# Kernel optimization log

Hardware: AMD Instinct MI355X
Metric: run time of the kernel (lower is better)

## Reference

```python
import jax, jax.numpy as jnp
import numpy as np

B, S, D, H = 4, 1024, 1024, 16
HD = D // H  # head_dim = 64


def setup_inputs() -> dict:
    key = jax.random.key(0)
    ks = jax.random.split(key, 9)
    scale = jnp.float32(1.0 / np.sqrt(D))
    w = lambda k: jax.random.normal(k, (D, D), jnp.float32) * scale
    return {
        "x": jax.random.normal(ks[0], (B, S, D), jnp.float32),
        "Wq_r": w(ks[1]), "Wq_i": w(ks[2]),
        "Wk_r": w(ks[3]), "Wk_i": w(ks[4]),
        "Wv_r": w(ks[5]), "Wv_i": w(ks[6]),
        "Wo_r": w(ks[7]), "Wo_i": w(ks[8]),
        "mask": jnp.ones((B, S, S), dtype=bool),
    }


def reference(x, Wq_r, Wq_i, Wk_r, Wk_i, Wv_r, Wv_i, Wo_r, Wo_i, mask):
    # Optical encoding: magnitude * exp(i * angle(x + i*roll(x,1,-1)))
    mag = jnp.abs(x)
    phase = jnp.arctan2(jnp.roll(x, 1, axis=-1), x)  # angle(x + i*rolled)
    opt = (mag * jnp.cos(phase)) + 1j * (mag * jnp.sin(phase))  # complex64 [B,S,D]

    Wq = Wq_r + 1j * Wq_i
    Wk = Wk_r + 1j * Wk_i
    Wv = Wv_r + 1j * Wv_i
    Wo = Wo_r + 1j * Wo_i

    def heads(t):  # [B,S,D] -> [B,H,S,HD]
        return jnp.transpose(t.reshape(B, S, H, HD), (0, 2, 1, 3))

    Q = heads(opt @ Wq)
    K = heads(opt @ Wk)
    V = heads(opt @ Wv)

    # Photonic correlation: abs of complex dot Q . conj(K)
    corr = jnp.einsum('bhqd,bhkd->bhqk', Q, jnp.conj(K))
    scores = jnp.abs(corr) / jnp.sqrt(jnp.float32(HD))
    scores = jnp.where(mask[:, None, :, :], scores, -jnp.inf)
    attn = jax.nn.softmax(scores, axis=-1)  # real weights [B,H,S,S]

    out = jnp.einsum('bhqk,bhkd->bhqd', attn.astype(V.dtype), V)  # complex
    out = jnp.transpose(out, (0, 2, 1, 3)).reshape(B, S, D)
    return jnp.real(out @ Wo)
```

## Files before the change

### kernel.cpp

```cpp
#include <hip/hip_runtime.h>
#include <hip/hip_bf16.h>


#define BB 4
#define SS 1024
#define DD 1024
#define HH 16
#define HD 64

typedef _Float16 f16x8 __attribute__((ext_vector_type(8)));
typedef _Float16 f16x4 __attribute__((ext_vector_type(4)));
typedef float    f32x4 __attribute__((ext_vector_type(4)));
typedef int      i32x2 __attribute__((ext_vector_type(2)));
typedef unsigned int u32x4 __attribute__((ext_vector_type(4)));

#define LOG2E 1.44269504f
#define C8S 0.18033688f

__global__ __launch_bounds__(256) void k_encode_h(const float* __restrict__ x,
                                                  _Float16* __restrict__ ore,
                                                  _Float16* __restrict__ oim) {
    const int g   = blockIdx.x * 256 + threadIdx.x;
    const int row = g >> 8;
    const int d0  = (g & 255) * 4;
    const float* xr = x + (size_t)row * DD;
    const float4 xc = *(const float4*)(xr + d0);
    const float xp0 = xr[(d0 + DD - 1) & (DD - 1)];
    const float cv[4] = {xc.x, xc.y, xc.z, xc.w};
    const float pv[4] = {xp0, xc.x, xc.y, xc.z};
    f16x4 hr, hi;
    #pragma unroll
    for (int j = 0; j < 4; ++j) {
        const float r2 = cv[j]*cv[j] + pv[j]*pv[j];
        float re = 0.f, im = 0.f;
        if (r2 > 1e-30f) {
            const float inv = rsqrtf(r2);
            const float mag = fabsf(cv[j]);
            re = mag * cv[j] * inv;
            im = mag * pv[j] * inv;
        }
        hr[j] = (_Float16)re; hi[j] = (_Float16)im;
    }
    *(f16x4*)(ore + (size_t)row*DD + d0) = hr;
    *(f16x4*)(oim + (size_t)row*DD + d0) = hi;
}

__global__ __launch_bounds__(256) void k_transw8(
    const float* w0, const float* w1, const float* w2, const float* w3,
    const float* w4, const float* w5, const float* w6, const float* w7,
    _Float16* wt)
{
    __shared__ _Float16 tile[64][68];
    const float* W;
    switch (blockIdx.z) {
        case 0: W = w0; break; case 1: W = w1; break;
        case 2: W = w2; break; case 3: W = w3; break;
        case 4: W = w4; break; case 5: W = w5; break;
        case 6: W = w6; break; default: W = w7; break;
    }
    _Float16* Wt = wt + (size_t)blockIdx.z * (1u << 20);
    const int t = threadIdx.x;
    const int r = t >> 4, c4 = (t & 15) * 4;
    const int gx = blockIdx.x * 64, gy = blockIdx.y * 64;
    #pragma unroll
    for (int rr = 0; rr < 4; ++rr) {
        const float4 v = *(const float4*)(W + (size_t)(gy + r + rr*16)*DD + gx + c4);
        tile[r + rr*16][c4+0] = (_Float16)v.x;
        tile[r + rr*16][c4+1] = (_Float16)v.y;
        tile[r + rr*16][c4+2] = (_Float16)v.z;
        tile[r + rr*16][c4+3] = (_Float16)v.w;
    }
    __syncthreads();
    #pragma unroll
    for (int rr = 0; rr < 4; ++rr) {
        const int n = r + rr*16;
        f16x4 o;
        o[0] = tile[c4+0][n]; o[1] = tile[c4+1][n];
        o[2] = tile[c4+2][n]; o[3] = tile[c4+3][n];
        *(f16x4*)(Wt + (size_t)(gx + n)*DD + gy + c4) = o;
    }
}

template<int MODE>
__global__ __launch_bounds__(256, 2) void k_cgemm_h(
    const _Float16* __restrict__ Ar, const _Float16* __restrict__ Ai,
    const _Float16* __restrict__ Btr, const _Float16* __restrict__ Bti,
    _Float16* __restrict__ Cr, _Float16* __restrict__ Ci, float* __restrict__ Cf)
{
    __shared__ _Float16 lds[2][4][4096];

    const int t = threadIdx.x, w = t >> 6, l = t & 63;
    const int lr = l & 15, lg = l >> 4;

    int wg = blockIdx.x;
    wg = (wg & 7) * 32 + (wg >> 3);
    const int m0 = (wg >> 3) * 128;
    const int n0 = (wg & 7) * 128;
    const int wr = w >> 1, wc = w & 1;

    const _Float16* gbase = (w == 0) ? Ar : (w == 1) ? Ai : (w == 2) ? Btr : Bti;
    const int rowbase = (w < 2) ? m0 : n0;
    const _Float16* gp = gbase + (size_t)(rowbase + (l >> 2)) * 1024 + (l & 3) * 8;

    #define GSTAGE(K0_, BUF_)                                                         \
        {                                                                             \
            _Float16* lb = &lds[BUF_][w][0];                                          \
            _Pragma("unroll")                                                         \
            for (int i = 0; i < 8; ++i)                                               \
                __builtin_amdgcn_global_load_lds(                                     \
                    (const __attribute__((address_space(1))) void*)                   \
                        (gp + (size_t)i*16*1024 + (K0_)),                             \
                    (__attribute__((address_space(3))) void*)(lb + i*512), 16, 0, 0); \
        }

    f32x4 accR[4][4] = {};
    f32x4 accI[4][4] = {};

    GSTAGE(0, 0);
    int cur = 0;

    for (int kt = 0; kt < 32; ++kt) {
        if (kt < 31) {
            GSTAGE((kt + 1) * 32, cur ^ 1);
            asm volatile("s_waitcnt vmcnt(8)" ::: "memory");
        } else {
            asm volatile("s_waitcnt vmcnt(0)" ::: "memory");
        }
        __builtin_amdgcn_s_barrier();
        __builtin_amdgcn_sched_barrier(0);

        const _Float16* lA = &lds[cur][0][0] + (wr*64 + lr)*32 + lg*8;
        const _Float16* lB = &lds[cur][2][0] + (wc*64 + lr)*32 + lg*8;

        f16x8 ar[4], ai[4], br[4], bi[4], nai[4];
        #pragma unroll
        for (int i = 0; i < 4; ++i) {
            ar[i] = *(const f16x8*)(lA + i*512);
            ai[i] = *(const f16x8*)(lA + 4096 + i*512);
            br[i] = *(const f16x8*)(lB + i*512);
            bi[i] = *(const f16x8*)(lB + 4096 + i*512);
            union { f16x8 h; u32x4 u; } nx;
            nx.h = ai[i]; nx.u ^= 0x80008000u; nai[i] = nx.h;
        }
        __builtin_amdgcn_s_setprio(1);
        #pragma unroll
        for (int i = 0; i < 4; ++i) {
            #pragma unroll
            for (int j = 0; j < 4; ++j) {
                accR[i][j] = __builtin_amdgcn_mfma_f32_16x16x32_f16(ar[i],  br[j], accR[i][j], 0, 0, 0);
                accR[i][j] = __builtin_amdgcn_mfma_f32_16x16x32_f16(nai[i], bi[j], accR[i][j], 0, 0, 0);
                if (MODE == 0) {
                    accI[i][j] = __builtin_amdgcn_mfma_f32_16x16x32_f16(ar[i], bi[j], accI[i][j], 0, 0, 0);
                    accI[i][j] = __builtin_amdgcn_mfma_f32_16x16x32_f16(ai[i], br[j], accI[i][j], 0, 0, 0);
                }
            }
        }
        __builtin_amdgcn_s_setprio(0);
        __builtin_amdgcn_sched_barrier(0);
        __builtin_amdgcn_s_barrier();
        cur ^= 1;
    }

    #pragma unroll
    for (int i = 0; i < 4; ++i) {
        #pragma unroll
        for (int j = 0; j < 4; ++j) {
            const int m = m0 + wr*64 + i*16 + lg*4;
            const int n = n0 + wc*64 + j*16 + lr;
            #pragma unroll
            for (int r = 0; r < 4; ++r) {
                if (MODE == 0) {
                    Cr[(size_t)(m + r)*1024 + n] = (_Float16)accR[i][j][r];
                    Ci[(size_t)(m + r)*1024 + n] = (_Float16)accI[i][j][r];
                } else {
                    Cf[(size_t)(m + r)*1024 + n] = accR[i][j][r];
                }
            }
        }
    }
}

#define QB 64
#define KT 32

__global__ __launch_bounds__(256, 4) void k_attn6(
    const _Float16* Qre, const _Float16* Qim,
    const _Float16* __restrict__ Kre, const _Float16* __restrict__ Kim,
    const _Float16* __restrict__ Vre, const _Float16* __restrict__ Vim,
    _Float16* Ore, _Float16* Oim)
{
    __shared__ __align__(16) _Float16 lds[2][4][2048];

    const int t = threadIdx.x, w = t >> 6, l = t & 63;
    const int lr = l & 15, lg = l >> 4;
    const int bh = blockIdx.x;
    const int h = bh & (HH - 1), b = bh >> 4;
    const int qw = blockIdx.y * QB + w * 16;

    const size_t kvbase = ((size_t)(b * SS)) * DD + h * HD;

    f16x8 qr[2], qi[2], nqr[2];
    {
        const size_t qoff = ((size_t)(b*SS + qw + lr)) * DD + h*HD + lg*8;
        #pragma unroll
        for (int ks = 0; ks < 2; ++ks) {
            qr[ks] = *(const f16x8*)(Qre + qoff + 32*ks);
            qi[ks] = *(const f16x8*)(Qim + qoff + 32*ks);
            union { f16x8 h; u32x4 u; } nx;
            nx.h = qr[ks]; nx.u ^= 0x80008000u; nqr[ks] = nx.h;
        }
    }

    const _Float16* gsrc;
    if (w < 2)
        gsrc = ((w == 0) ? Kre : Kim) + kvbase + (size_t)(l >> 3) * DD + ((l & 7) ^ (l >> 3)) * 8;
    else
        gsrc = ((w == 2) ? Vre : Vim) + kvbase + (size_t)(l >> 1) * DD + (l & 1) * 8;

    #define STAGE(KT_, BUF_)                                                          \
        {                                                                             \
            _Float16* lb = &lds[BUF_][w][0];                                          \
            if (w < 2) {                                                              \
                _Pragma("unroll")                                                     \
                for (int i = 0; i < 4; ++i)                                           \
                    __builtin_amdgcn_global_load_lds(                                 \
                        (const __attribute__((address_space(1))) void*)               \
                            (gsrc + (size_t)((KT_)*KT + 8*i) * DD),                   \
                        (__attribute__((address_space(3))) void*)(lb + i*512),        \
                        16, 0, 0);                                                    \
            } else {                                                                  \
                _Pragma("unroll")                                                     \
                for (int i = 0; i < 4; ++i)                                           \
                    __builtin_amdgcn_global_load_lds(                                 \
                        (const __attribute__((address_space(1))) void*)               \
                            (gsrc + (size_t)((KT_)*KT) * DD + i*16),                  \
                        (__attribute__((address_space(3))) void*)(lb + i*512),        \
                        16, 0, 0);                                                    \
            }                                                                         \
        }

    f32x4 o_re[4] = {}, o_im[4] = {};
    float m_s  = 32.f;
    float m2_s = 1024.f;
    float mC_s = -32.f * C8S;
    float l_l  = 0.f;

    STAGE(0, 0);
    int cur = 0;

    for (int kt = 0; kt < SS/KT; ++kt) {
        if (kt < SS/KT - 1) {
            STAGE(kt + 1, cur ^ 1);
            asm volatile("s_waitcnt vmcnt(4)" ::: "memory");
        } else {
            asm volatile("s_waitcnt vmcnt(0)" ::: "memory");
        }
        __builtin_amdgcn_s_barrier();
        __builtin_amdgcn_sched_barrier(0);

        const _Float16* Kr_s = &lds[cur][0][0];
        const _Float16* Ki_s = &lds[cur][1][0];

        f32x4 dre[2] = {}, dim_[2] = {};
        #pragma unroll
        for (int st = 0; st < 2; ++st) {
            const int row = st*16 + lr;
            #pragma unroll
            for (int ks = 0; ks < 2; ++ks) {
                const int c = ((4*ks + lg) ^ (lr & 7)) * 8;
                const f16x8 kr = *(const f16x8*)(Kr_s + row*64 + c);
                const f16x8 ki = *(const f16x8*)(Ki_s + row*64 + c);
                dre[st]  = __builtin_amdgcn_mfma_f32_16x16x32_f16(kr, qr[ks],  dre[st],  0, 0, 0);
                dre[st]  = __builtin_amdgcn_mfma_f32_16x16x32_f16(ki, qi[ks],  dre[st],  0, 0, 0);
                dim_[st] = __builtin_amdgcn_mfma_f32_16x16x32_f16(kr, qi[ks],  dim_[st], 0, 0, 0);
                dim_[st] = __builtin_amdgcn_mfma_f32_16x16x32_f16(ki, nqr[ks], dim_[st], 0, 0, 0);
            }
        }

        f16x4 pa[2];
        {
            float d2[2][4];
            float t2 = 0.f;
            #pragma unroll
            for (int st = 0; st < 2; ++st)
                #pragma unroll
                for (int r = 0; r < 4; ++r) {
                    d2[st][r] = fmaf(dre[st][r], dre[st][r],
                                     dim_[st][r] * dim_[st][r]);
                    t2 = fmaxf(t2, d2[st][r]);
                }
            if (!__all(t2 <= m2_s)) {
                float tm;
                asm("v_sqrt_f32 %0, %1" : "=v"(tm) : "v"(t2));
                tm = fmaxf(tm, __shfl_xor(tm, 16));
                tm = fmaxf(tm, __shfl_xor(tm, 32));
                const float mn = fmaxf(m_s, tm);
                const float ce = (m_s - mn) * C8S;
                float cq;
                asm("v_exp_f32 %0, %1" : "=v"(cq) : "v"(ce));
                l_l *= cq;
                f32x4 cT;
                #pragma unroll
                for (int r = 0; r < 4; ++r) cT[r] = __shfl(cq, lg*4 + r);
                #pragma unroll
                for (int d = 0; d < 4; ++d) { o_re[d] *= cT; o_im[d] *= cT; }
                m_s  = mn;
                m2_s = mn * mn;
                mC_s = -mn * C8S;
            }
            float ls = 0.f;
            #pragma unroll
            for (int st = 0; st < 2; ++st)
                #pragma unroll
                for (int r = 0; r < 4; ++r) {
                    float u, p;
                    asm("v_sqrt_f32 %0, %1" : "=v"(u) : "v"(d2[st][r]));
                    const float e = fmaf(u, C8S, mC_s);
                    asm("v_exp_f32 %0, %1" : "=v"(p) : "v"(e));
                    pa[st][r] = (_Float16)p;
                    ls += p;
                }
            l_l += ls;
        }

        const unsigned vrb = (unsigned)(uintptr_t)&lds[cur][2][0] + 8u*l;
        const unsigned vib = (unsigned)(uintptr_t)&lds[cur][3][0] + 8u*l;
        i32x2 fr[2][2], fi[2][2];
        #pragma unroll
        for (int st = 0; st < 2; ++st) {
            asm volatile("ds_read_b64_tr_b16 %0, %1" : "=v"(fr[0][st]) : "v"(vrb + st*512u) : "memory");
            asm volatile("ds_read_b64_tr_b16 %0, %1" : "=v"(fi[0][st]) : "v"(vib + st*512u) : "memory");
        }
        #pragma unroll
        for (int d = 0; d < 4; ++d) {
            const int cb = d & 1, nb = cb ^ 1;
            if (d < 3) {
                #pragma unroll
                for (int st = 0; st < 2; ++st) {
                    asm volatile("ds_read_b64_tr_b16 %0, %1" : "=v"(fr[nb][st]) : "v"(vrb + (d+1)*1024u + st*512u) : "memory");
                    asm volatile("ds_read_b64_tr_b16 %0, %1" : "=v"(fi[nb][st]) : "v"(vib + (d+1)*1024u + st*512u) : "memory");
                }
                asm volatile("s_waitcnt lgkmcnt(4)" ::: "memory");
            } else {
                asm volatile("s_waitcnt lgkmcnt(0)" ::: "memory");
            }
            __builtin_amdgcn_sched_barrier(0);
            __builtin_amdgcn_s_setprio(1);
            #pragma unroll
            for (int st = 0; st < 2; ++st) {
                union { i32x2 i; f16x4 h; } cr_, ci_;
                cr_.i = fr[cb][st]; ci_.i = fi[cb][st];
                o_re[d] = __builtin_amdgcn_mfma_f32_16x16x16f16(pa[st], cr_.h, o_re[d], 0, 0, 0);
                o_im[d] = __builtin_amdgcn_mfma_f32_16x16x16f16(pa[st], ci_.h, o_im[d], 0, 0, 0);
            }
            __builtin_amdgcn_s_setprio(0);
        }

        __builtin_amdgcn_sched_barrier(0);
        __builtin_amdgcn_s_barrier();
        cur ^= 1;
    }

    {
        float lq = l_l;
        lq += __shfl_xor(lq, 16);
        lq += __shfl_xor(lq, 32);
        const float inv = 1.f / lq;
        f32x4 iT;
        #pragma unroll
        for (int r = 0; r < 4; ++r) iT[r] = __shfl(inv, lg*4 + r);
        #pragma unroll
        for (int d = 0; d < 4; ++d)
            #pragma unroll
            for (int r = 0; r < 4; ++r) {
                const size_t row = (size_t)(b*SS + qw + lg*4 + r);
                Ore[row*DD + h*HD + d*16 + lr] = (_Float16)(o_re[d][r] * iT[r]);
                Oim[row*DD + h*HD + d*16 + lr] = (_Float16)(o_im[d][r] * iT[r]);
            }
    }
}

extern "C" void kernel_launch(void* const* d_in, const int* in_sizes, int n_in,
                              void* d_out, int out_size, void* d_ws, size_t ws_size,
                              hipStream_t stream) {
    const float* x   = (const float*)d_in[0];
    const float* Wqr = (const float*)d_in[1];
    const float* Wqi = (const float*)d_in[2];
    const float* Wkr = (const float*)d_in[3];
    const float* Wki = (const float*)d_in[4];
    const float* Wvr = (const float*)d_in[5];
    const float* Wvi = (const float*)d_in[6];
    const float* Wor = (const float*)d_in[7];
    const float* Woi = (const float*)d_in[8];

    const size_t P  = (size_t)BB * SS * DD;
    const size_t WP = 1u << 20;
    if (ws_size < (8 * P + 8 * WP) * sizeof(_Float16)) return;

    _Float16* wh   = (_Float16*)d_ws;
    _Float16* optR = wh;
    _Float16* optI = wh + P;
    _Float16* Qr = wh + 2*P; _Float16* Qi = wh + 3*P;
    _Float16* Kr = wh + 4*P; _Float16* Ki = wh + 5*P;
    _Float16* Vr = wh + 6*P; _Float16* Vi = wh + 7*P;
    _Float16* W8 = wh + 8*P;

    k_encode_h<<<(int)(P / 1024), 256, 0, stream>>>(x, optR, optI);
    k_transw8<<<dim3(16, 16, 8), 256, 0, stream>>>(Wqr, Wqi, Wkr, Wki, Wvr, Wvi, Wor, Woi, W8);

    k_cgemm_h<0><<<256, 256, 0, stream>>>(optR, optI, W8 + 0*WP, W8 + 1*WP, Qr, Qi, nullptr);
    k_cgemm_h<0><<<256, 256, 0, stream>>>(optR, optI, W8 + 2*WP, W8 + 3*WP, Kr, Ki, nullptr);
    k_cgemm_h<0><<<256, 256, 0, stream>>>(optR, optI, W8 + 4*WP, W8 + 5*WP, Vr, Vi, nullptr);

    k_attn6<<<dim3(BB * HH, SS / QB, 1), 256, 0, stream>>>(Qr, Qi, Kr, Ki, Vr, Vi, Qr, Qi);

    k_cgemm_h<1><<<256, 256, 0, stream>>>(Qr, Qi, W8 + 6*WP, W8 + 7*WP,
                                          nullptr, nullptr, (float*)d_out);
}
```

Before: 242.2 us.

## Fuse QKV GEMMs into one launch and split attention over key halves

The three Q/K/V complex GEMM launches are merged into one 768-block launch that picks the weight matrix from the block index. Attention is split along the key dimension into two halves (grid z=2), doubling the block count for better CU occupancy. Each half writes unnormalised partial outputs plus row max and sum, and a new combine kernel merges them with log-sum-exp rescaling. The output GEMM becomes its own kernel specialised for the real part. The cost is extra workspace, an extra launch, and more fp16 partial-output traffic, with some precision risk from storing unnormalised partials in fp16.

```diff
diff --git a/kernel.cpp b/kernel.cpp
--- a/kernel.cpp
+++ b/kernel.cpp
@@ -81,22 +81,29 @@
     }
 }
 
-template<int MODE>
-__global__ __launch_bounds__(256, 2) void k_cgemm_h(
+__global__ __launch_bounds__(256, 2) void k_cgemm_qkv(
     const _Float16* __restrict__ Ar, const _Float16* __restrict__ Ai,
-    const _Float16* __restrict__ Btr, const _Float16* __restrict__ Bti,
-    _Float16* __restrict__ Cr, _Float16* __restrict__ Ci, float* __restrict__ Cf)
+    const _Float16* __restrict__ W8, _Float16* __restrict__ CQ)
 {
     __shared__ _Float16 lds[2][4][4096];
 
     const int t = threadIdx.x, w = t >> 6, l = t & 63;
     const int lr = l & 15, lg = l >> 4;
+    const size_t P  = (size_t)BB * SS * DD;
+    const size_t WP = 1u << 20;
 
     int wg = blockIdx.x;
-    wg = (wg & 7) * 32 + (wg >> 3);
-    const int m0 = (wg >> 3) * 128;
-    const int n0 = (wg & 7) * 128;
+    wg = (wg & 7) * 96 + (wg >> 3);
+    const int mt  = wg / 24, nt = wg % 24;
+    const int m0  = mt * 128;
+    const int mat = nt >> 3;
+    const int n0  = (nt & 7) * 128;
     const int wr = w >> 1, wc = w & 1;
+
+    const _Float16* Btr = W8 + (size_t)mat * 2 * WP;
+    const _Float16* Bti = Btr + WP;
+    _Float16* Cr = CQ + (size_t)mat * 2 * P;
+    _Float16* Ci = Cr + P;
 
     const _Float16* gbase = (w == 0) ? Ar : (w == 1) ? Ai : (w == 2) ? Btr : Bti;
     const int rowbase = (w < 2) ? m0 : n0;
@@ -149,10 +156,8 @@
             for (int j = 0; j < 4; ++j) {
                 accR[i][j] = __builtin_amdgcn_mfma_f32_16x16x32_f16(ar[i],  br[j], accR[i][j], 0, 0, 0);
                 accR[i][j] = __builtin_amdgcn_mfma_f32_16x16x32_f16(nai[i], bi[j], accR[i][j], 0, 0, 0);
-                if (MODE == 0) {
-                    accI[i][j] = __builtin_amdgcn_mfma_f32_16x16x32_f16(ar[i], bi[j], accI[i][j], 0, 0, 0);
-                    accI[i][j] = __builtin_amdgcn_mfma_f32_16x16x32_f16(ai[i], br[j], accI[i][j], 0, 0, 0);
-                }
+                accI[i][j] = __builtin_amdgcn_mfma_f32_16x16x32_f16(ar[i],  bi[j], accI[i][j], 0, 0, 0);
+                accI[i][j] = __builtin_amdgcn_mfma_f32_16x16x32_f16(ai[i],  br[j], accI[i][j], 0, 0, 0);
             }
         }
         __builtin_amdgcn_s_setprio(0);
@@ -169,13 +174,85 @@
             const int n = n0 + wc*64 + j*16 + lr;
             #pragma unroll
             for (int r = 0; r < 4; ++r) {
-                if (MODE == 0) {
-                    Cr[(size_t)(m + r)*1024 + n] = (_Float16)accR[i][j][r];
-                    Ci[(size_t)(m + r)*1024 + n] = (_Float16)accI[i][j][r];
-                } else {
-                    Cf[(size_t)(m + r)*1024 + n] = accR[i][j][r];
-                }
-            }
+                Cr[(size_t)(m + r)*1024 + n] = (_Float16)accR[i][j][r];
+                Ci[(size_t)(m + r)*1024 + n] = (_Float16)accI[i][j][r];
+            }
+        }
+    }
+}
+
+__global__ __launch_bounds__(256, 2) void k_cgemm_o(
+    const _Float16* __restrict__ Ar, const _Float16* __restrict__ Ai,
+    const _Float16* __restrict__ Btr, const _Float16* __restrict__ Bti,
+    float* __restrict__ Cf)
+{
+    __shared__ _Float16 lds[2][4][4096];
+
+    const int t = threadIdx.x, w = t >> 6, l = t & 63;
+    const int lr = l & 15, lg = l >> 4;
+
+    int wg = blockIdx.x;
+    wg = (wg & 7) * 32 + (wg >> 3);
+    const int m0 = (wg >> 3) * 128;
+    const int n0 = (wg & 7) * 128;
+    const int wr = w >> 1, wc = w & 1;
+
+    const _Float16* gbase = (w == 0) ? Ar : (w == 1) ? Ai : (w == 2) ? Btr : Bti;
+    const int rowbase = (w < 2) ? m0 : n0;
+    const _Float16* gp = gbase + (size_t)(rowbase + (l >> 2)) * 1024 + (l & 3) * 8;
+
+    f32x4 accR[4][4] = {};
+
+    GSTAGE(0, 0);
+    int cur = 0;
+
+    for (int kt = 0; kt < 32; ++kt) {
+        if (kt < 31) {
+            GSTAGE((kt + 1) * 32, cur ^ 1);
+            asm volatile("s_waitcnt vmcnt(8)" ::: "memory");
+        } else {
+            asm volatile("s_waitcnt vmcnt(0)" ::: "memory");
+        }
+        __builtin_amdgcn_s_barrier();
+        __builtin_amdgcn_sched_barrier(0);
+
+        const _Float16* lA = &lds[cur][0][0] + (wr*64 + lr)*32 + lg*8;
+        const _Float16* lB = &lds[cur][2][0] + (wc*64 + lr)*32 + lg*8;
+
+        f16x8 ar[4], br[4], bi[4], nai[4];
+        #pragma unroll
+        for (int i = 0; i < 4; ++i) {
+            ar[i] = *(const f16x8*)(lA + i*512);
+            f16x8 aiv = *(const f16x8*)(lA + 4096 + i*512);
+            br[i] = *(const f16x8*)(lB + i*512);
+            bi[i] = *(const f16x8*)(lB + 4096 + i*512);
+            union { f16x8 h; u32x4 u; } nx;
+            nx.h = aiv; nx.u ^= 0x80008000u; nai[i] = nx.h;
+        }
+        __builtin_amdgcn_s_setprio(1);
+        #pragma unroll
+        for (int i = 0; i < 4; ++i) {
+            #pragma unroll
+            for (int j = 0; j < 4; ++j) {
+                accR[i][j] = __builtin_amdgcn_mfma_f32_16x16x32_f16(ar[i],  br[j], accR[i][j], 0, 0, 0);
+                accR[i][j] = __builtin_amdgcn_mfma_f32_16x16x32_f16(nai[i], bi[j], accR[i][j], 0, 0, 0);
+            }
+        }
+        __builtin_amdgcn_s_setprio(0);
+        __builtin_amdgcn_sched_barrier(0);
+        __builtin_amdgcn_s_barrier();
+        cur ^= 1;
+    }
+
+    #pragma unroll
+    for (int i = 0; i < 4; ++i) {
+        #pragma unroll
+        for (int j = 0; j < 4; ++j) {
+            const int m = m0 + wr*64 + i*16 + lg*4;
+            const int n = n0 + wc*64 + j*16 + lr;
+            #pragma unroll
+            for (int r = 0; r < 4; ++r)
+                Cf[(size_t)(m + r)*1024 + n] = accR[i][j][r];
         }
     }
 }
@@ -183,11 +260,11 @@
 #define QB 64
 #define KT 32
 
-__global__ __launch_bounds__(256, 4) void k_attn6(
-    const _Float16* Qre, const _Float16* Qim,
+__global__ __launch_bounds__(256, 4) void k_attn7(
+    const _Float16* __restrict__ Qre, const _Float16* __restrict__ Qim,
     const _Float16* __restrict__ Kre, const _Float16* __restrict__ Kim,
     const _Float16* __restrict__ Vre, const _Float16* __restrict__ Vim,
-    _Float16* Ore, _Float16* Oim)
+    _Float16* __restrict__ PO, float* __restrict__ Lb, float* __restrict__ Mb)
 {
     __shared__ __align__(16) _Float16 lds[2][4][2048];
 
@@ -196,6 +273,11 @@
     const int bh = blockIdx.x;
     const int h = bh & (HH - 1), b = bh >> 4;
     const int qw = blockIdx.y * QB + w * 16;
+    const int z  = blockIdx.z;
+    const int kt0 = z * 16, kt1 = kt0 + 16;
+    const size_t PLANE = (size_t)BB * SS * DD;
+    _Float16* Por = PO + (size_t)z * 2 * PLANE;
+    _Float16* Poi = Por + PLANE;
 
     const size_t kvbase = ((size_t)(b * SS)) * DD + h * HD;
 
@@ -245,11 +327,11 @@
     float mC_s = -32.f * C8S;
     float l_l  = 0.f;
 
-    STAGE(0, 0);
+    STAGE(kt0, 0);
     int cur = 0;
 
-    for (int kt = 0; kt < SS/KT; ++kt) {
-        if (kt < SS/KT - 1) {
+    for (int kt = kt0; kt < kt1; ++kt) {
+        if (kt < kt1 - 1) {
             STAGE(kt + 1, cur ^ 1);
             asm volatile("s_waitcnt vmcnt(4)" ::: "memory");
         } else {
@@ -365,19 +447,52 @@
         float lq = l_l;
         lq += __shfl_xor(lq, 16);
         lq += __shfl_xor(lq, 32);
-        const float inv = 1.f / lq;
-        f32x4 iT;
-        #pragma unroll
-        for (int r = 0; r < 4; ++r) iT[r] = __shfl(inv, lg*4 + r);
+        if (l < 16) {
+            const int q = qw + lr;
+            Lb[z * 65536 + (bh << 10) + q] = lq;
+            Mb[z * 65536 + (bh << 10) + q] = m_s;
+        }
         #pragma unroll
         for (int d = 0; d < 4; ++d)
             #pragma unroll
             for (int r = 0; r < 4; ++r) {
                 const size_t row = (size_t)(b*SS + qw + lg*4 + r);
-                Ore[row*DD + h*HD + d*16 + lr] = (_Float16)(o_re[d][r] * iT[r]);
-                Oim[row*DD + h*HD + d*16 + lr] = (_Float16)(o_im[d][r] * iT[r]);
-            }
-    }
+                Por[row*DD + h*HD + d*16 + lr] = (_Float16)o_re[d][r];
+                Poi[row*DD + h*HD + d*16 + lr] = (_Float16)o_im[d][r];
+            }
+    }
+}
+
+__global__ __launch_bounds__(256) void k_combine(
+    const _Float16* __restrict__ P0r, const _Float16* __restrict__ P0i,
+    const _Float16* __restrict__ P1r, const _Float16* __restrict__ P1i,
+    const float* __restrict__ Lb, const float* __restrict__ Mb,
+    _Float16* __restrict__ Or, _Float16* __restrict__ Oi)
+{
+    const int u = blockIdx.x * 256 + threadIdx.x;
+    const int row = u >> 7;
+    const int c8  = u & 127;
+    const int hh  = c8 >> 3;
+    const int q = row & 1023, b = row >> 10;
+    const int li = ((b * 16 + hh) << 10) + q;
+    const float l0 = Lb[li], l1 = Lb[65536 + li];
+    const float m0 = Mb[li], m1 = Mb[65536 + li];
+    const float mm = fmaxf(m0, m1);
+    const float f0 = exp2f((m0 - mm) * C8S);
+    const float f1 = exp2f((m1 - mm) * C8S);
+    const float inv = 1.f / fmaf(l0, f0, l1 * f1);
+    const float s0 = f0 * inv, s1 = f1 * inv;
+    const size_t off = (size_t)row * DD + c8 * 8;
+    const f16x8 a0 = *(const f16x8*)(P0r + off), a1 = *(const f16x8*)(P1r + off);
+    const f16x8 b0 = *(const f16x8*)(P0i + off), b1 = *(const f16x8*)(P1i + off);
+    f16x8 xr, xi;
+    #pragma unroll
+    for (int j = 0; j < 8; ++j) {
+        xr[j] = (_Float16)fmaf((float)a0[j], s0, (float)a1[j] * s1);
+        xi[j] = (_Float16)fmaf((float)b0[j], s0, (float)b1[j] * s1);
+    }
+    *(f16x8*)(Or + off) = xr;
+    *(f16x8*)(Oi + off) = xi;
 }
 
 extern "C" void kernel_launch(void* const* d_in, const int* in_sizes, int n_in,
@@ -395,7 +510,8 @@
 
     const size_t P  = (size_t)BB * SS * DD;
     const size_t WP = 1u << 20;
-    if (ws_size < (8 * P + 8 * WP) * sizeof(_Float16)) return;
+    const size_t need = (12 * P + 8 * WP) * sizeof(_Float16) + 4ull * 4 * 65536;
+    if (ws_size < need) return;
 
     _Float16* wh   = (_Float16*)d_ws;
     _Float16* optR = wh;
@@ -404,16 +520,21 @@
     _Float16* Kr = wh + 4*P; _Float16* Ki = wh + 5*P;
     _Float16* Vr = wh + 6*P; _Float16* Vi = wh + 7*P;
     _Float16* W8 = wh + 8*P;
+    _Float16* PO = wh + 8*P + 8*WP;
+    float*    LM = (float*)(wh + 12*P + 8*WP);
+    float*    Lb = LM;
+    float*    Mb = LM + 131072;
 
     k_encode_h<<<(int)(P / 1024), 256, 0, stream>>>(x, optR, optI);
     k_transw8<<<dim3(16, 16, 8), 256, 0, stream>>>(Wqr, Wqi, Wkr, Wki, Wvr, Wvi, Wor, Woi, W8);
 
-    k_cgemm_h<0><<<256, 256, 0, stream>>>(optR, optI, W8 + 0*WP, W8 + 1*WP, Qr, Qi, nullptr);
-    k_cgemm_h<0><<<256, 256, 0, stream>>>(optR, optI, W8 + 2*WP, W8 + 3*WP, Kr, Ki, nullptr);
-    k_cgemm_h<0><<<256, 256, 0, stream>>>(optR, optI, W8 + 4*WP, W8 + 5*WP, Vr, Vi, nullptr);
-
-    k_attn6<<<dim3(BB * HH, SS / QB, 1), 256, 0, stream>>>(Qr, Qi, Kr, Ki, Vr, Vi, Qr, Qi);
-
-    k_cgemm_h<1><<<256, 256, 0, stream>>>(Qr, Qi, W8 + 6*WP, W8 + 7*WP,
-                                          nullptr, nullptr, (float*)d_out);
-}
+    k_cgemm_qkv<<<768, 256, 0, stream>>>(optR, optI, W8, Qr);
+
+    k_attn7<<<dim3(BB * HH, SS / QB, 2), 256, 0, stream>>>(
+        Qr, Qi, Kr, Ki, Vr, Vi, PO, Lb, Mb);
+
+    k_combine<<<2048, 256, 0, stream>>>(PO, PO + P, PO + 2*P, PO + 3*P,
+                                        Lb, Mb, Qr, Qi);
+
+    k_cgemm_o<<<256, 256, 0, stream>>>(Qr, Qi, W8 + 6*WP, W8 + 7*WP, (float*)d_out);
+}
```

Result: faster. 228.7 us (-5.6%).

## Split attention over two KV halves with combine kernel; merge prep kernels

Applied to the files above, without the earlier changes.

Attention is now split along the key dimension into two halves (grid z=2). Each half writes unnormalized partial outputs plus row sums and maxima, and a new combine kernel rescales and merges the two halves before the output projection. This doubles the number of attention blocks, which raises occupancy on a grid that was only 1024 blocks. The cost is extra partial-output traffic, one more launch and more workspace. The encode and weight-transpose kernels are also fused into one launch to save launch overhead.

```diff
diff --git a/kernel.cpp b/kernel.cpp
--- a/kernel.cpp
+++ b/kernel.cpp
@@ -17,67 +17,69 @@
 #define LOG2E 1.44269504f
 #define C8S 0.18033688f
 
-__global__ __launch_bounds__(256) void k_encode_h(const float* __restrict__ x,
-                                                  _Float16* __restrict__ ore,
-                                                  _Float16* __restrict__ oim) {
-    const int g   = blockIdx.x * 256 + threadIdx.x;
-    const int row = g >> 8;
-    const int d0  = (g & 255) * 4;
-    const float* xr = x + (size_t)row * DD;
-    const float4 xc = *(const float4*)(xr + d0);
-    const float xp0 = xr[(d0 + DD - 1) & (DD - 1)];
-    const float cv[4] = {xc.x, xc.y, xc.z, xc.w};
-    const float pv[4] = {xp0, xc.x, xc.y, xc.z};
-    f16x4 hr, hi;
-    #pragma unroll
-    for (int j = 0; j < 4; ++j) {
-        const float r2 = cv[j]*cv[j] + pv[j]*pv[j];
-        float re = 0.f, im = 0.f;
-        if (r2 > 1e-30f) {
-            const float inv = rsqrtf(r2);
-            const float mag = fabsf(cv[j]);
-            re = mag * cv[j] * inv;
-            im = mag * pv[j] * inv;
-        }
-        hr[j] = (_Float16)re; hi[j] = (_Float16)im;
-    }
-    *(f16x4*)(ore + (size_t)row*DD + d0) = hr;
-    *(f16x4*)(oim + (size_t)row*DD + d0) = hi;
-}
-
-__global__ __launch_bounds__(256) void k_transw8(
+__global__ __launch_bounds__(256) void k_prep(
+    const float* __restrict__ x,
     const float* w0, const float* w1, const float* w2, const float* w3,
     const float* w4, const float* w5, const float* w6, const float* w7,
-    _Float16* wt)
+    _Float16* __restrict__ ore, _Float16* __restrict__ oim,
+    _Float16* __restrict__ wt)
 {
     __shared__ _Float16 tile[64][68];
-    const float* W;
-    switch (blockIdx.z) {
-        case 0: W = w0; break; case 1: W = w1; break;
-        case 2: W = w2; break; case 3: W = w3; break;
-        case 4: W = w4; break; case 5: W = w5; break;
-        case 6: W = w6; break; default: W = w7; break;
-    }
-    _Float16* Wt = wt + (size_t)blockIdx.z * (1u << 20);
     const int t = threadIdx.x;
-    const int r = t >> 4, c4 = (t & 15) * 4;
-    const int gx = blockIdx.x * 64, gy = blockIdx.y * 64;
-    #pragma unroll
-    for (int rr = 0; rr < 4; ++rr) {
-        const float4 v = *(const float4*)(W + (size_t)(gy + r + rr*16)*DD + gx + c4);
-        tile[r + rr*16][c4+0] = (_Float16)v.x;
-        tile[r + rr*16][c4+1] = (_Float16)v.y;
-        tile[r + rr*16][c4+2] = (_Float16)v.z;
-        tile[r + rr*16][c4+3] = (_Float16)v.w;
-    }
-    __syncthreads();
-    #pragma unroll
-    for (int rr = 0; rr < 4; ++rr) {
-        const int n = r + rr*16;
-        f16x4 o;
-        o[0] = tile[c4+0][n]; o[1] = tile[c4+1][n];
-        o[2] = tile[c4+2][n]; o[3] = tile[c4+3][n];
-        *(f16x4*)(Wt + (size_t)(gx + n)*DD + gy + c4) = o;
+
+    if (blockIdx.z < 8) {
+        const float* W;
+        switch (blockIdx.z) {
+            case 0: W = w0; break; case 1: W = w1; break;
+            case 2: W = w2; break; case 3: W = w3; break;
+            case 4: W = w4; break; case 5: W = w5; break;
+            case 6: W = w6; break; default: W = w7; break;
+        }
+        _Float16* Wt = wt + (size_t)blockIdx.z * (1u << 20);
+        const int r = t >> 4, c4 = (t & 15) * 4;
+        const int gx = blockIdx.x * 64, gy = blockIdx.y * 64;
+        #pragma unroll
+        for (int rr = 0; rr < 4; ++rr) {
+            const float4 v = *(const float4*)(W + (size_t)(gy + r + rr*16)*DD + gx + c4);
+            tile[r + rr*16][c4+0] = (_Float16)v.x;
+            tile[r + rr*16][c4+1] = (_Float16)v.y;
+            tile[r + rr*16][c4+2] = (_Float16)v.z;
+            tile[r + rr*16][c4+3] = (_Float16)v.w;
+        }
+        __syncthreads();
+        #pragma unroll
+        for (int rr = 0; rr < 4; ++rr) {
+            const int n = r + rr*16;
+            f16x4 o;
+            o[0] = tile[c4+0][n]; o[1] = tile[c4+1][n];
+            o[2] = tile[c4+2][n]; o[3] = tile[c4+3][n];
+            *(f16x4*)(Wt + (size_t)(gx + n)*DD + gy + c4) = o;
+        }
+    } else {
+        const int bid = (blockIdx.z - 8) * 256 + blockIdx.y * 16 + blockIdx.x;
+        const int g   = bid * 256 + t;
+        const int row = g >> 8;
+        const int d0  = (g & 255) * 4;
+        const float* xr = x + (size_t)row * DD;
+        const float4 xc = *(const float4*)(xr + d0);
+        const float xp0 = xr[(d0 + DD - 1) & (DD - 1)];
+        const float cv[4] = {xc.x, xc.y, xc.z, xc.w};
+        const float pv[4] = {xp0, xc.x, xc.y, xc.z};
+        f16x4 hr, hi;
+        #pragma unroll
+        for (int j = 0; j < 4; ++j) {
+            const float r2 = cv[j]*cv[j] + pv[j]*pv[j];
+            float re = 0.f, im = 0.f;
+            if (r2 > 1e-30f) {
+                const float inv = rsqrtf(r2);
+                const float mag = fabsf(cv[j]);
+                re = mag * cv[j] * inv;
+                im = mag * pv[j] * inv;
+            }
+            hr[j] = (_Float16)re; hi[j] = (_Float16)im;
+        }
+        *(f16x4*)(ore + (size_t)row*DD + d0) = hr;
+        *(f16x4*)(oim + (size_t)row*DD + d0) = hi;
     }
 }
 
@@ -183,11 +185,11 @@
 #define QB 64
 #define KT 32
 
-__global__ __launch_bounds__(256, 4) void k_attn6(
-    const _Float16* Qre, const _Float16* Qim,
+__global__ __launch_bounds__(256, 4) void k_attn7(
+    const _Float16* __restrict__ Qre, const _Float16* __restrict__ Qim,
     const _Float16* __restrict__ Kre, const _Float16* __restrict__ Kim,
     const _Float16* __restrict__ Vre, const _Float16* __restrict__ Vim,
-    _Float16* Ore, _Float16* Oim)
+    _Float16* __restrict__ PO, float* __restrict__ Lb, float* __restrict__ Mb)
 {
     __shared__ __align__(16) _Float16 lds[2][4][2048];
 
@@ -196,6 +198,11 @@
     const int bh = blockIdx.x;
     const int h = bh & (HH - 1), b = bh >> 4;
     const int qw = blockIdx.y * QB + w * 16;
+    const int z  = blockIdx.z;
+    const int kt0 = z * 16, kt1 = kt0 + 16;
+    const size_t PLANE = (size_t)BB * SS * DD;
+    _Float16* Por = PO + (size_t)z * 2 * PLANE;
+    _Float16* Poi = Por + PLANE;
 
     const size_t kvbase = ((size_t)(b * SS)) * DD + h * HD;
 
@@ -217,7 +224,7 @@
     else
         gsrc = ((w == 2) ? Vre : Vim) + kvbase + (size_t)(l >> 1) * DD + (l & 1) * 8;
 
-    #define STAGE(KT_, BUF_)                                                          \
+    #define ASTAGE(KT_, BUF_)                                                         \
         {                                                                             \
             _Float16* lb = &lds[BUF_][w][0];                                          \
             if (w < 2) {                                                              \
@@ -245,12 +252,12 @@
     float mC_s = -32.f * C8S;
     float l_l  = 0.f;
 
-    STAGE(0, 0);
+    ASTAGE(kt0, 0);
     int cur = 0;
 
-    for (int kt = 0; kt < SS/KT; ++kt) {
-        if (kt < SS/KT - 1) {
-            STAGE(kt + 1, cur ^ 1);
+    for (int kt = kt0; kt < kt1; ++kt) {
+        if (kt < kt1 - 1) {
+            ASTAGE(kt + 1, cur ^ 1);
             asm volatile("s_waitcnt vmcnt(4)" ::: "memory");
         } else {
             asm volatile("s_waitcnt vmcnt(0)" ::: "memory");
@@ -365,19 +372,52 @@
         float lq = l_l;
         lq += __shfl_xor(lq, 16);
         lq += __shfl_xor(lq, 32);
-        const float inv = 1.f / lq;
-        f32x4 iT;
-        #pragma unroll
-        for (int r = 0; r < 4; ++r) iT[r] = __shfl(inv, lg*4 + r);
+        if (l < 16) {
+            const int q = qw + lr;
+            Lb[z * 65536 + (bh << 10) + q] = lq;
+            Mb[z * 65536 + (bh << 10) + q] = m_s;
+        }
         #pragma unroll
         for (int d = 0; d < 4; ++d)
             #pragma unroll
             for (int r = 0; r < 4; ++r) {
                 const size_t row = (size_t)(b*SS + qw + lg*4 + r);
-                Ore[row*DD + h*HD + d*16 + lr] = (_Float16)(o_re[d][r] * iT[r]);
-                Oim[row*DD + h*HD + d*16 + lr] = (_Float16)(o_im[d][r] * iT[r]);
-            }
-    }
+                Por[row*DD + h*HD + d*16 + lr] = (_Float16)o_re[d][r];
+                Poi[row*DD + h*HD + d*16 + lr] = (_Float16)o_im[d][r];
+            }
+    }
+}
+
+__global__ __launch_bounds__(256) void k_combine(
+    const _Float16* __restrict__ P0r, const _Float16* __restrict__ P0i,
+    const _Float16* __restrict__ P1r, const _Float16* __restrict__ P1i,
+    const float* __restrict__ Lb, const float* __restrict__ Mb,
+    _Float16* __restrict__ Or, _Float16* __restrict__ Oi)
+{
+    const int u = blockIdx.x * 256 + threadIdx.x;
+    const int row = u >> 7;
+    const int c8  = u & 127;
+    const int hh  = c8 >> 3;
+    const int q = row & 1023, b = row >> 10;
+    const int li = ((b * 16 + hh) << 10) + q;
+    const float l0 = Lb[li], l1 = Lb[65536 + li];
+    const float m0 = Mb[li], m1 = Mb[65536 + li];
+    const float mm = fmaxf(m0, m1);
+    const float f0 = exp2f((m0 - mm) * C8S);
+    const float f1 = exp2f((m1 - mm) * C8S);
+    const float inv = 1.f / fmaf(l0, f0, l1 * f1);
+    const float s0 = f0 * inv, s1 = f1 * inv;
+    const size_t off = (size_t)row * DD + c8 * 8;
+    const f16x8 a0 = *(const f16x8*)(P0r + off), a1 = *(const f16x8*)(P1r + off);
+    const f16x8 b0 = *(const f16x8*)(P0i + off), b1 = *(const f16x8*)(P1i + off);
+    f16x8 xr, xi;
+    #pragma unroll
+    for (int j = 0; j < 8; ++j) {
+        xr[j] = (_Float16)fmaf((float)a0[j], s0, (float)a1[j] * s1);
+        xi[j] = (_Float16)fmaf((float)b0[j], s0, (float)b1[j] * s1);
+    }
+    *(f16x8*)(Or + off) = xr;
+    *(f16x8*)(Oi + off) = xi;
 }
 
 extern "C" void kernel_launch(void* const* d_in, const int* in_sizes, int n_in,
@@ -395,7 +435,8 @@
 
     const size_t P  = (size_t)BB * SS * DD;
     const size_t WP = 1u << 20;
-    if (ws_size < (8 * P + 8 * WP) * sizeof(_Float16)) return;
+    const size_t need = (12 * P + 8 * WP) * sizeof(_Float16) + 4ull * 4 * 65536;
+    if (ws_size < need) return;
 
     _Float16* wh   = (_Float16*)d_ws;
     _Float16* optR = wh;
@@ -404,15 +445,23 @@
     _Float16* Kr = wh + 4*P; _Float16* Ki = wh + 5*P;
     _Float16* Vr = wh + 6*P; _Float16* Vi = wh + 7*P;
     _Float16* W8 = wh + 8*P;
-
-    k_encode_h<<<(int)(P / 1024), 256, 0, stream>>>(x, optR, optI);
-    k_transw8<<<dim3(16, 16, 8), 256, 0, stream>>>(Wqr, Wqi, Wkr, Wki, Wvr, Wvi, Wor, Woi, W8);
+    _Float16* PO = wh + 8*P + 8*WP;
+    float*    LM = (float*)(wh + 12*P + 8*WP);
+    float*    Lb = LM;
+    float*    Mb = LM + 131072;
+
+    k_prep<<<dim3(16, 16, 24), 256, 0, stream>>>(
+        x, Wqr, Wqi, Wkr, Wki, Wvr, Wvi, Wor, Woi, optR, optI, W8);
 
     k_cgemm_h<0><<<256, 256, 0, stream>>>(optR, optI, W8 + 0*WP, W8 + 1*WP, Qr, Qi, nullptr);
     k_cgemm_h<0><<<256, 256, 0, stream>>>(optR, optI, W8 + 2*WP, W8 + 3*WP, Kr, Ki, nullptr);
     k_cgemm_h<0><<<256, 256, 0, stream>>>(optR, optI, W8 + 4*WP, W8 + 5*WP, Vr, Vi, nullptr);
 
-    k_attn6<<<dim3(BB * HH, SS / QB, 1), 256, 0, stream>>>(Qr, Qi, Kr, Ki, Vr, Vi, Qr, Qi);
+    k_attn7<<<dim3(BB * HH, SS / QB, 2), 256, 0, stream>>>(
+        Qr, Qi, Kr, Ki, Vr, Vi, PO, Lb, Mb);
+
+    k_combine<<<2048, 256, 0, stream>>>(PO, PO + P, PO + 2*P, PO + 3*P,
+                                        Lb, Mb, Qr, Qi);
 
     k_cgemm_h<1><<<256, 256, 0, stream>>>(Qr, Qi, W8 + 6*WP, W8 + 7*WP,
                                           nullptr, nullptr, (float*)d_out);
```

Result: slower. 251.4 us (+3.8%).

## Merge QKV projections into one launch and load B operands directly to registers

Applied to the files above, without the earlier changes.

The three Q/K/V complex GEMM launches become a single 768-block launch. Each block picks its weight matrix and output from its tile index, with a swizzle that groups blocks sharing the same A rows. Inside the GEMM, only the A operand is staged through LDS with async global-to-LDS copies, which halves LDS use. The B operand (transposed weights) is now loaded straight from global memory into double-buffered registers one step ahead. This removes launch gaps and improves A-tile reuse across the three weights, at the cost of more VGPR pressure and uncached-by-LDS B loads that could stall the MFMA loop.

```diff
diff --git a/kernel.cpp b/kernel.cpp
--- a/kernel.cpp
+++ b/kernel.cpp
@@ -82,83 +82,125 @@
 }
 
 template<int MODE>
-__global__ __launch_bounds__(256, 2) void k_cgemm_h(
+__global__ __launch_bounds__(256, 2) void k_cgemm_bd(
     const _Float16* __restrict__ Ar, const _Float16* __restrict__ Ai,
-    const _Float16* __restrict__ Btr, const _Float16* __restrict__ Bti,
-    _Float16* __restrict__ Cr, _Float16* __restrict__ Ci, float* __restrict__ Cf)
+    const _Float16* __restrict__ W8, _Float16* __restrict__ CQ,
+    float* __restrict__ Cf)
 {
-    __shared__ _Float16 lds[2][4][4096];
+    __shared__ _Float16 lds[2][2][4096];
 
     const int t = threadIdx.x, w = t >> 6, l = t & 63;
     const int lr = l & 15, lg = l >> 4;
-
-    int wg = blockIdx.x;
-    wg = (wg & 7) * 32 + (wg >> 3);
-    const int m0 = (wg >> 3) * 128;
-    const int n0 = (wg & 7) * 128;
+    const size_t P  = (size_t)BB * SS * DD;
+    const size_t WP = 1u << 20;
+
+    int m0, n0;
+    const _Float16* Btr;
+    const _Float16* Bti;
+    _Float16* Cr = nullptr; _Float16* Ci = nullptr;
+    if (MODE == 0) {
+        int wg = blockIdx.x;
+        wg = (wg & 7) * 96 + (wg >> 3);
+        const int mt = wg / 24, nt = wg % 24;
+        m0 = mt * 128;
+        const int mat = nt >> 3;
+        n0 = (nt & 7) * 128;
+        Btr = W8 + (size_t)mat * 2 * WP;
+        Bti = Btr + WP;
+        Cr = CQ + (size_t)mat * 2 * P;
+        Ci = Cr + P;
+    } else {
+        int wg = blockIdx.x;
+        wg = (wg & 7) * 32 + (wg >> 3);
+        m0 = (wg >> 3) * 128;
+        n0 = (wg & 7) * 128;
+        Btr = W8 + (size_t)6 * WP;
+        Bti = Btr + WP;
+    }
     const int wr = w >> 1, wc = w & 1;
 
-    const _Float16* gbase = (w == 0) ? Ar : (w == 1) ? Ai : (w == 2) ? Btr : Bti;
-    const int rowbase = (w < 2) ? m0 : n0;
-    const _Float16* gp = gbase + (size_t)(rowbase + (l >> 2)) * 1024 + (l & 3) * 8;
-
-    #define GSTAGE(K0_, BUF_)                                                         \
+    const _Float16* gsrc = ((w < 2) ? Ar : Ai)
+        + (size_t)(m0 + (w & 1) * 64 + (l >> 2)) * 1024 + (l & 3) * 8;
+    const int aseg = (w >> 1);
+    const int arow0 = (w & 1) * 64;
+
+    #define ASTG(K0_, BUF_)                                                           \
         {                                                                             \
-            _Float16* lb = &lds[BUF_][w][0];                                          \
+            _Float16* lb = &lds[BUF_][aseg][arow0 * 32];                              \
             _Pragma("unroll")                                                         \
-            for (int i = 0; i < 8; ++i)                                               \
+            for (int i = 0; i < 4; ++i)                                               \
                 __builtin_amdgcn_global_load_lds(                                     \
                     (const __attribute__((address_space(1))) void*)                   \
-                        (gp + (size_t)i*16*1024 + (K0_)),                             \
+                        (gsrc + (size_t)i*16*1024 + (K0_)),                           \
                     (__attribute__((address_space(3))) void*)(lb + i*512), 16, 0, 0); \
+        }
+
+    const size_t bbase = (size_t)(n0 + wc*64 + lr) * 1024 + lg * 8;
+
+    #define BLOAD(K0_, BR_, BI_)                                                      \
+        {                                                                             \
+            _Pragma("unroll")                                                         \
+            for (int j = 0; j < 4; ++j) {                                             \
+                const size_t o = bbase + (size_t)j*16*1024 + (K0_);                   \
+                BR_[j] = *(const f16x8*)(Btr + o);                                    \
+                BI_[j] = *(const f16x8*)(Bti + o);                                    \
+            }                                                                         \
         }
 
     f32x4 accR[4][4] = {};
     f32x4 accI[4][4] = {};
-
-    GSTAGE(0, 0);
-    int cur = 0;
-
-    for (int kt = 0; kt < 32; ++kt) {
-        if (kt < 31) {
-            GSTAGE((kt + 1) * 32, cur ^ 1);
-            asm volatile("s_waitcnt vmcnt(8)" ::: "memory");
-        } else {
-            asm volatile("s_waitcnt vmcnt(0)" ::: "memory");
-        }
-        __builtin_amdgcn_s_barrier();
-        __builtin_amdgcn_sched_barrier(0);
-
-        const _Float16* lA = &lds[cur][0][0] + (wr*64 + lr)*32 + lg*8;
-        const _Float16* lB = &lds[cur][2][0] + (wc*64 + lr)*32 + lg*8;
-
-        f16x8 ar[4], ai[4], br[4], bi[4], nai[4];
-        #pragma unroll
-        for (int i = 0; i < 4; ++i) {
-            ar[i] = *(const f16x8*)(lA + i*512);
-            ai[i] = *(const f16x8*)(lA + 4096 + i*512);
-            br[i] = *(const f16x8*)(lB + i*512);
-            bi[i] = *(const f16x8*)(lB + 4096 + i*512);
-            union { f16x8 h; u32x4 u; } nx;
-            nx.h = ai[i]; nx.u ^= 0x80008000u; nai[i] = nx.h;
-        }
-        __builtin_amdgcn_s_setprio(1);
-        #pragma unroll
-        for (int i = 0; i < 4; ++i) {
-            #pragma unroll
-            for (int j = 0; j < 4; ++j) {
-                accR[i][j] = __builtin_amdgcn_mfma_f32_16x16x32_f16(ar[i],  br[j], accR[i][j], 0, 0, 0);
-                accR[i][j] = __builtin_amdgcn_mfma_f32_16x16x32_f16(nai[i], bi[j], accR[i][j], 0, 0, 0);
-                if (MODE == 0) {
-                    accI[i][j] = __builtin_amdgcn_mfma_f32_16x16x32_f16(ar[i], bi[j], accI[i][j], 0, 0, 0);
-                    accI[i][j] = __builtin_amdgcn_mfma_f32_16x16x32_f16(ai[i], br[j], accI[i][j], 0, 0, 0);
-                }
-            }
-        }
-        __builtin_amdgcn_s_setprio(0);
-        __builtin_amdgcn_sched_barrier(0);
-        __builtin_amdgcn_s_barrier();
-        cur ^= 1;
+    f16x8 br0[4], bi0[4], br1[4], bi1[4];
+
+    ASTG(0, 0);
+    BLOAD(0, br0, bi0);
+
+    #define PHASE(KT_, CBUF_, NBUF_, BRC_, BIC_, BRN_, BIN_)                          \
+        {                                                                             \
+            if ((KT_) < 31) {                                                         \
+                ASTG(((KT_) + 1) * 32, NBUF_);                                        \
+                asm volatile("s_waitcnt vmcnt(4)" ::: "memory");                      \
+            } else {                                                                  \
+                asm volatile("s_waitcnt vmcnt(0)" ::: "memory");                      \
+            }                                                                         \
+            __builtin_amdgcn_s_barrier();                                             \
+            __builtin_amdgcn_sched_barrier(0);                                        \
+            if ((KT_) < 31) BLOAD(((KT_) + 1) * 32, BRN_, BIN_);                      \
+            const _Float16* lA = &lds[CBUF_][0][0] + (wr*64 + lr)*32 + lg*8;          \
+            f16x8 ar_[4], nai_[4];                                                    \
+            f16x8 ai_[4];                                                             \
+            _Pragma("unroll")                                                         \
+            for (int i = 0; i < 4; ++i) {                                             \
+                ar_[i] = *(const f16x8*)(lA + i*512);                                 \
+                ai_[i] = *(const f16x8*)(lA + 4096 + i*512);                          \
+                union { f16x8 h; u32x4 u; } nx;                                       \
+                nx.h = ai_[i]; nx.u ^= 0x80008000u; nai_[i] = nx.h;                   \
+            }                                                                         \
+            __builtin_amdgcn_s_setprio(1);                                            \
+            _Pragma("unroll")                                                         \
+            for (int i = 0; i < 4; ++i) {                                             \
+                _Pragma("unroll")                                                     \
+                for (int j = 0; j < 4; ++j) {                                         \
+                    accR[i][j] = __builtin_amdgcn_mfma_f32_16x16x32_f16(              \
+                        ar_[i], BRC_[j], accR[i][j], 0, 0, 0);                        \
+                    accR[i][j] = __builtin_amdgcn_mfma_f32_16x16x32_f16(              \
+                        nai_[i], BIC_[j], accR[i][j], 0, 0, 0);                       \
+                    if (MODE == 0) {                                                  \
+                        accI[i][j] = __builtin_amdgcn_mfma_f32_16x16x32_f16(          \
+                            ar_[i], BIC_[j], accI[i][j], 0, 0, 0);                    \
+                        accI[i][j] = __builtin_amdgcn_mfma_f32_16x16x32_f16(          \
+                            ai_[i], BRC_[j], accI[i][j], 0, 0, 0);                    \
+                    }                                                                 \
+                }                                                                     \
+            }                                                                         \
+            __builtin_amdgcn_s_setprio(0);                                            \
+            __builtin_amdgcn_sched_barrier(0);                                        \
+            __builtin_amdgcn_s_barrier();                                             \
+        }
+
+    #pragma unroll 1
+    for (int kt = 0; kt < 32; kt += 2) {
+        PHASE(kt,     0, 1, br0, bi0, br1, bi1);
+        PHASE(kt + 1, 1, 0, br1, bi1, br0, bi0);
     }
 
     #pragma unroll
@@ -217,7 +259,7 @@
     else
         gsrc = ((w == 2) ? Vre : Vim) + kvbase + (size_t)(l >> 1) * DD + (l & 1) * 8;
 
-    #define STAGE(KT_, BUF_)                                                          \
+    #define ASTAGE(KT_, BUF_)                                                         \
         {                                                                             \
             _Float16* lb = &lds[BUF_][w][0];                                          \
             if (w < 2) {                                                              \
@@ -245,12 +287,12 @@
     float mC_s = -32.f * C8S;
     float l_l  = 0.f;
 
-    STAGE(0, 0);
+    ASTAGE(0, 0);
     int cur = 0;
 
     for (int kt = 0; kt < SS/KT; ++kt) {
         if (kt < SS/KT - 1) {
-            STAGE(kt + 1, cur ^ 1);
+            ASTAGE(kt + 1, cur ^ 1);
             asm volatile("s_waitcnt vmcnt(4)" ::: "memory");
         } else {
             asm volatile("s_waitcnt vmcnt(0)" ::: "memory");
@@ -408,12 +450,9 @@
     k_encode_h<<<(int)(P / 1024), 256, 0, stream>>>(x, optR, optI);
     k_transw8<<<dim3(16, 16, 8), 256, 0, stream>>>(Wqr, Wqi, Wkr, Wki, Wvr, Wvi, Wor, Woi, W8);
 
-    k_cgemm_h<0><<<256, 256, 0, stream>>>(optR, optI, W8 + 0*WP, W8 + 1*WP, Qr, Qi, nullptr);
-    k_cgemm_h<0><<<256, 256, 0, stream>>>(optR, optI, W8 + 2*WP, W8 + 3*WP, Kr, Ki, nullptr);
-    k_cgemm_h<0><<<256, 256, 0, stream>>>(optR, optI, W8 + 4*WP, W8 + 5*WP, Vr, Vi, nullptr);
+    k_cgemm_bd<0><<<768, 256, 0, stream>>>(optR, optI, W8, Qr, nullptr);
 
     k_attn6<<<dim3(BB * HH, SS / QB, 1), 256, 0, stream>>>(Qr, Qi, Kr, Ki, Vr, Vi, Qr, Qi);
 
-    k_cgemm_h<1><<<256, 256, 0, stream>>>(Qr, Qi, W8 + 6*WP, W8 + 7*WP,
-                                          nullptr, nullptr, (float*)d_out);
+    k_cgemm_bd<1><<<256, 256, 0, stream>>>(Qr, Qi, W8, nullptr, (float*)d_out);
 }
```

New measurement: 266.6 us. +10.1%, slower.
